# Optimization experiments

Measured on AMD Instinct MI355X. Metric: run time of the kernel, lower is better.

The kernel has to match this reference:

```python
import jax, jax.numpy as jnp
import numpy as np

B, N, D, C = 256, 256, 512, 1024
EPS = 1e-12  # F.normalize eps


def _l2norm(x):
    n = jnp.linalg.norm(x, axis=-1, keepdims=True)
    return x / jnp.maximum(n, EPS)


def setup_inputs() -> dict:
    key = jax.random.key(0)
    k1, k2, k3 = jax.random.split(key, 3)
    return {
        "image_tokens": jax.random.normal(k1, (B, N, D), dtype=jnp.float32),
        "text_features": jax.random.normal(k2, (C, D), dtype=jnp.float32),
        "log_tau": jnp.asarray(np.log(0.07), dtype=jnp.float32),
        "log_attn_tau": jnp.asarray(np.log(0.07), dtype=jnp.float32),
        "pid_labels": jax.random.randint(k3, (B,), 0, C),
    }


def reference(image_tokens, text_features, log_tau, log_attn_tau, pid_labels):
    toks = _l2norm(image_tokens.astype(jnp.float32))        # [B,N,D]
    txt = _l2norm(text_features.astype(jnp.float32))        # [C,D]
    sims = jnp.einsum('bnd,cd->bnc', toks, txt)             # [B,N,C]
    gt = pid_labels.astype(jnp.int32)
    # sims[arange(B), :, gt] -> [B,N]
    sims_gt = jnp.take_along_axis(sims, gt[:, None, None], axis=2)[..., 0]
    attn_tau = jnp.clip(jnp.exp(log_attn_tau), 0.01, 1.0)
    w = jax.nn.softmax(sims_gt / attn_tau, axis=1)          # [B,N]
    logits = jnp.einsum('bn,bnc->bc', w, sims)              # [B,C]
    tau = jnp.clip(jnp.exp(log_tau), 0.01, 1.0)
    logits = logits / tau
    # cross_entropy with label_smoothing=0.0, mean reduction
    logp = jax.nn.log_softmax(logits, axis=-1)
    nll = -jnp.take_along_axis(logp, gt[:, None], axis=1)[:, 0]
    return jnp.mean(nll)
```

## Files before the change

### kernel.cpp

```cpp
#include <hip/hip_runtime.h>
#include <math.h>

#define Bb 256
#define Nn 256
#define Dd 512
#define Cc 1024
#define KC 8
#define KD (Dd / KC)
#define PR 16
#define PSTR 516

__device__ __forceinline__ float waveReduceSum(float v) {
    #pragma unroll
    for (int off = 32; off > 0; off >>= 1)
        v += __shfl_xor(v, off, 64);
    return v;
}
__device__ __forceinline__ float waveReduceMax(float v) {
    #pragma unroll
    for (int off = 32; off > 0; off >>= 1)
        v = fmaxf(v, __shfl_xor(v, off, 64));
    return v;
}

__global__ void k_prep(const float* __restrict__ txt, float* __restrict__ txt_t,
                       float* __restrict__ invc) {
    __shared__ float tile[PR * PSTR];
    __shared__ float invs[PR];
    const int c0 = blockIdx.x * PR;
    const int tid = threadIdx.x;
    #pragma unroll
    for (int i = tid; i < PR * 128; i += 256) {
        const int r = i >> 7, c4 = i & 127;
        const float4 v = *(const float4*)(txt + (size_t)(c0 + r) * Dd + c4 * 4);
        *(float4*)&tile[r * PSTR + c4 * 4] = v;
    }
    __syncthreads();
    {
        const int r = tid >> 4, k = tid & 15;
        float s = 0.f;
        #pragma unroll
        for (int i = 0; i < 32; ++i) {
            const float x = tile[r * PSTR + i * 16 + k];
            s = fmaf(x, x, s);
        }
        s += __shfl_xor(s, 1, 64);
        s += __shfl_xor(s, 2, 64);
        s += __shfl_xor(s, 4, 64);
        s += __shfl_xor(s, 8, 64);
        if (k == 0) {
            const float inv = 1.0f / fmaxf(sqrtf(s), 1e-12f);
            invs[r] = inv;
            invc[c0 + r] = inv;
        }
    }
    __syncthreads();
    {
        const int c = tid & 15;
        const int d0 = tid >> 4;
        const float inv = invs[c];
        #pragma unroll
        for (int d = d0; d < Dd; d += 16)
            txt_t[(size_t)d * Cc + c0 + c] = tile[c * PSTR + d] * inv;
    }
}

__global__ void __launch_bounds__(1024) k_attn_q(const float* __restrict__ toks,
                                                 const float* __restrict__ txt,
                                                 const float* __restrict__ invc,
                                                 const int* __restrict__ pid,
                                                 const float* __restrict__ log_attn_tau,
                                                 float* __restrict__ q) {
    const int b = blockIdx.x;
    const int tid = threadIdx.x;
    const int wv = tid >> 6;
    const int lane = tid & 63;
    __shared__ float xg[Dd];
    __shared__ float qpart_s[16][Dd];
    __shared__ float ms[16], Ss[16];
    const int g = pid[b];
    if (tid < Dd) xg[tid] = txt[(size_t)g * Dd + tid] * invc[g];
    __syncthreads();
    float at = expf(log_attn_tau[0]);
    at = fminf(fmaxf(at, 0.01f), 1.0f);
    const float iat = 1.0f / at;

    const float4 xg0 = *(const float4*)&xg[lane * 8];
    const float4 xg1 = *(const float4*)&xg[lane * 8 + 4];

    float m = -INFINITY, S = 0.0f;
    float qa[8] = {0.f, 0.f, 0.f, 0.f, 0.f, 0.f, 0.f, 0.f};

    const float* base = toks + ((size_t)b * Nn + wv * 16) * Dd + lane * 8;
    float4 t0 = *(const float4*)base;
    float4 t1 = *(const float4*)(base + 4);
    #pragma unroll 4
    for (int r = 0; r < 16; ++r) {
        float4 n0, n1;
        if (r < 15) {
            const float* p = base + (size_t)(r + 1) * Dd;
            n0 = *(const float4*)p;
            n1 = *(const float4*)(p + 4);
        }
        float dot = t0.x*xg0.x + t0.y*xg0.y + t0.z*xg0.z + t0.w*xg0.w
                  + t1.x*xg1.x + t1.y*xg1.y + t1.z*xg1.z + t1.w*xg1.w;
        float ss  = t0.x*t0.x + t0.y*t0.y + t0.z*t0.z + t0.w*t0.w
                  + t1.x*t1.x + t1.y*t1.y + t1.z*t1.z + t1.w*t1.w;
        dot = waveReduceSum(dot);
        ss = waveReduceSum(ss);
        const float inv = 1.0f / fmaxf(sqrtf(ss), 1e-12f);
        const float s = dot * inv;
        if (s > m) {
            const float sc = expf((m - s) * iat);
            S = S * sc + 1.0f;
            qa[0] = qa[0]*sc + inv*t0.x; qa[1] = qa[1]*sc + inv*t0.y;
            qa[2] = qa[2]*sc + inv*t0.z; qa[3] = qa[3]*sc + inv*t0.w;
            qa[4] = qa[4]*sc + inv*t1.x; qa[5] = qa[5]*sc + inv*t1.y;
            qa[6] = qa[6]*sc + inv*t1.z; qa[7] = qa[7]*sc + inv*t1.w;
            m = s;
        } else {
            const float e = expf((s - m) * iat);
            S += e;
            const float w = e * inv;
            qa[0] = fmaf(w, t0.x, qa[0]); qa[1] = fmaf(w, t0.y, qa[1]);
            qa[2] = fmaf(w, t0.z, qa[2]); qa[3] = fmaf(w, t0.w, qa[3]);
            qa[4] = fmaf(w, t1.x, qa[4]); qa[5] = fmaf(w, t1.y, qa[5]);
            qa[6] = fmaf(w, t1.z, qa[6]); qa[7] = fmaf(w, t1.w, qa[7]);
        }
        t0 = n0; t1 = n1;
    }
    #pragma unroll
    for (int j = 0; j < 8; ++j) qpart_s[wv][lane * 8 + j] = qa[j];
    if (lane == 0) { ms[wv] = m; Ss[wv] = S; }
    __syncthreads();
    if (tid < Dd) {
        float M = -INFINITY;
        #pragma unroll
        for (int w = 0; w < 16; ++w) M = fmaxf(M, ms[w]);
        float Stot = 0.f, acc = 0.f;
        #pragma unroll
        for (int w = 0; w < 16; ++w) {
            const float sc = expf((ms[w] - M) * iat);
            Stot = fmaf(Ss[w], sc, Stot);
            acc = fmaf(qpart_s[w][tid], sc, acc);
        }
        q[(size_t)b * Dd + tid] = acc / Stot;
    }
}

__global__ void k_logits(const float* __restrict__ q, const float* __restrict__ txt_t,
                         float* __restrict__ part) {
    const int b0 = blockIdx.x * 4;
    const int kc = blockIdx.y;
    const int d0 = kc * KD;
    const int t = threadIdx.x;
    __shared__ float qs[4][KD];
    {
        const int j = t >> 6, d = t & 63;
        qs[j][d] = q[(size_t)(b0 + j) * Dd + d0 + d];
    }
    __syncthreads();
    const float4* xt = (const float4*)txt_t;
    float4 a0 = {0,0,0,0}, a1 = {0,0,0,0}, a2 = {0,0,0,0}, a3 = {0,0,0,0};
    #pragma unroll 4
    for (int d = 0; d < KD; d += 4) {
        const float4 q0 = *(const float4*)&qs[0][d];
        const float4 q1 = *(const float4*)&qs[1][d];
        const float4 q2 = *(const float4*)&qs[2][d];
        const float4 q3 = *(const float4*)&qs[3][d];
        const float4 x0 = xt[(size_t)(d0 + d + 0) * (Cc / 4) + t];
        const float4 x1 = xt[(size_t)(d0 + d + 1) * (Cc / 4) + t];
        const float4 x2 = xt[(size_t)(d0 + d + 2) * (Cc / 4) + t];
        const float4 x3 = xt[(size_t)(d0 + d + 3) * (Cc / 4) + t];
        a0.x = fmaf(q0.x,x0.x,a0.x); a0.y = fmaf(q0.x,x0.y,a0.y); a0.z = fmaf(q0.x,x0.z,a0.z); a0.w = fmaf(q0.x,x0.w,a0.w);
        a0.x = fmaf(q0.y,x1.x,a0.x); a0.y = fmaf(q0.y,x1.y,a0.y); a0.z = fmaf(q0.y,x1.z,a0.z); a0.w = fmaf(q0.y,x1.w,a0.w);
        a0.x = fmaf(q0.z,x2.x,a0.x); a0.y = fmaf(q0.z,x2.y,a0.y); a0.z = fmaf(q0.z,x2.z,a0.z); a0.w = fmaf(q0.z,x2.w,a0.w);
        a0.x = fmaf(q0.w,x3.x,a0.x); a0.y = fmaf(q0.w,x3.y,a0.y); a0.z = fmaf(q0.w,x3.z,a0.z); a0.w = fmaf(q0.w,x3.w,a0.w);
        a1.x = fmaf(q1.x,x0.x,a1.x); a1.y = fmaf(q1.x,x0.y,a1.y); a1.z = fmaf(q1.x,x0.z,a1.z); a1.w = fmaf(q1.x,x0.w,a1.w);
        a1.x = fmaf(q1.y,x1.x,a1.x); a1.y = fmaf(q1.y,x1.y,a1.y); a1.z = fmaf(q1.y,x1.z,a1.z); a1.w = fmaf(q1.y,x1.w,a1.w);
        a1.x = fmaf(q1.z,x2.x,a1.x); a1.y = fmaf(q1.z,x2.y,a1.y); a1.z = fmaf(q1.z,x2.z,a1.z); a1.w = fmaf(q1.z,x2.w,a1.w);
        a1.x = fmaf(q1.w,x3.x,a1.x); a1.y = fmaf(q1.w,x3.y,a1.y); a1.z = fmaf(q1.w,x3.z,a1.z); a1.w = fmaf(q1.w,x3.w,a1.w);
        a2.x = fmaf(q2.x,x0.x,a2.x); a2.y = fmaf(q2.x,x0.y,a2.y); a2.z = fmaf(q2.x,x0.z,a2.z); a2.w = fmaf(q2.x,x0.w,a2.w);
        a2.x = fmaf(q2.y,x1.x,a2.x); a2.y = fmaf(q2.y,x1.y,a2.y); a2.z = fmaf(q2.y,x1.z,a2.z); a2.w = fmaf(q2.y,x1.w,a2.w);
        a2.x = fmaf(q2.z,x2.x,a2.x); a2.y = fmaf(q2.z,x2.y,a2.y); a2.z = fmaf(q2.z,x2.z,a2.z); a2.w = fmaf(q2.z,x2.w,a2.w);
        a2.x = fmaf(q2.w,x3.x,a2.x); a2.y = fmaf(q2.w,x3.y,a2.y); a2.z = fmaf(q2.w,x3.z,a2.z); a2.w = fmaf(q2.w,x3.w,a2.w);
        a3.x = fmaf(q3.x,x0.x,a3.x); a3.y = fmaf(q3.x,x0.y,a3.y); a3.z = fmaf(q3.x,x0.z,a3.z); a3.w = fmaf(q3.x,x0.w,a3.w);
        a3.x = fmaf(q3.y,x1.x,a3.x); a3.y = fmaf(q3.y,x1.y,a3.y); a3.z = fmaf(q3.y,x1.z,a3.z); a3.w = fmaf(q3.y,x1.w,a3.w);
        a3.x = fmaf(q3.z,x2.x,a3.x); a3.y = fmaf(q3.z,x2.y,a3.y); a3.z = fmaf(q3.z,x2.z,a3.z); a3.w = fmaf(q3.z,x2.w,a3.w);
        a3.x = fmaf(q3.w,x3.x,a3.x); a3.y = fmaf(q3.w,x3.y,a3.y); a3.z = fmaf(q3.w,x3.z,a3.z); a3.w = fmaf(q3.w,x3.w,a3.w);
    }
    float* pb = part + ((size_t)kc * Bb + b0) * Cc;
    ((float4*)(pb + 0 * Cc))[t] = a0;
    ((float4*)(pb + 1 * Cc))[t] = a1;
    ((float4*)(pb + 2 * Cc))[t] = a2;
    ((float4*)(pb + 3 * Cc))[t] = a3;
}

__global__ void k_lse(const float* __restrict__ part, const int* __restrict__ pid,
                      const float* __restrict__ log_tau, float* __restrict__ out) {
    const int b = blockIdx.x;
    const int t = threadIdx.x;
    float4 l = {0,0,0,0};
    #pragma unroll
    for (int kc = 0; kc < KC; ++kc) {
        const float4 p = ((const float4*)(part + ((size_t)kc * Bb + b) * Cc))[t];
        l.x += p.x; l.y += p.y; l.z += p.z; l.w += p.w;
    }
    float tau = expf(log_tau[0]);
    tau = fminf(fmaxf(tau, 0.01f), 1.0f);
    const float itau = 1.0f / tau;
    l.x *= itau; l.y *= itau; l.z *= itau; l.w *= itau;

    const int g = pid[b];
    __shared__ float redm[4], reds[4], sgt;
    if ((g >> 2) == t) {
        const float v[4] = {l.x, l.y, l.z, l.w};
        sgt = v[g & 3];
    }
    float m = fmaxf(fmaxf(l.x, l.y), fmaxf(l.z, l.w));
    m = waveReduceMax(m);
    if ((t & 63) == 0) redm[t >> 6] = m;
    __syncthreads();
    m = fmaxf(fmaxf(redm[0], redm[1]), fmaxf(redm[2], redm[3]));
    float e = expf(l.x - m) + expf(l.y - m) + expf(l.z - m) + expf(l.w - m);
    e = waveReduceSum(e);
    if ((t & 63) == 0) reds[t >> 6] = e;
    __syncthreads();
    if (t == 0) {
        const float S = reds[0] + reds[1] + reds[2] + reds[3];
        const float nll = m + logf(S) - sgt;
        atomicAdd(out, nll * (1.0f / (float)Bb));
    }
}

extern "C" void kernel_launch(void* const* d_in, const int* in_sizes, int n_in,
                              void* d_out, int out_size, void* d_ws, size_t ws_size,
                              hipStream_t stream) {
    const float* toks = (const float*)d_in[0];
    const float* txt = (const float*)d_in[1];
    const float* log_tau = (const float*)d_in[2];
    const float* log_attn_tau = (const float*)d_in[3];
    const int* pid = (const int*)d_in[4];
    float* out = (float*)d_out;

    float* ws = (float*)d_ws;
    float* txt_t = ws;
    float* invc  = txt_t + (size_t)Dd * Cc;
    float* q     = invc + Cc;
    float* part  = q + (size_t)Bb * Dd;

    hipMemsetAsync(out, 0, sizeof(float), stream);
    k_prep<<<Cc / PR, 256, 0, stream>>>(txt, txt_t, invc);
    k_attn_q<<<Bb, 1024, 0, stream>>>(toks, txt, invc, pid, log_attn_tau, q);
    k_logits<<<dim3(Bb / 4, KC), 256, 0, stream>>>(q, txt_t, part);
    k_lse<<<Bb, 256, 0, stream>>>(part, pid, log_tau, out);
}
```

Before: 222.6 us.

## Split attention pooling across two blocks per batch and decouple from text prep

```diff
diff --git a/kernel.cpp b/kernel.cpp
--- a/kernel.cpp
+++ b/kernel.cpp
@@ -7,7 +7,7 @@
 #define Cc 1024
 #define KC 8
 #define KD (Dd / KC)
-#define PR 16
+#define PR 32
 #define PSTR 516
 
 __device__ __forceinline__ float waveReduceSum(float v) {
@@ -23,8 +23,7 @@
     return v;
 }
 
-__global__ void k_prep(const float* __restrict__ txt, float* __restrict__ txt_t,
-                       float* __restrict__ invc) {
+__global__ void k_prep(const float* __restrict__ txt, float* __restrict__ txt_t) {
     __shared__ float tile[PR * PSTR];
     __shared__ float invs[PR];
     const int c0 = blockIdx.x * PR;
@@ -37,50 +36,56 @@
     }
     __syncthreads();
     {
-        const int r = tid >> 4, k = tid & 15;
+        const int r = tid >> 3, k = tid & 7;
         float s = 0.f;
         #pragma unroll
-        for (int i = 0; i < 32; ++i) {
-            const float x = tile[r * PSTR + i * 16 + k];
+        for (int i = 0; i < 64; ++i) {
+            const float x = tile[r * PSTR + i * 8 + k];
             s = fmaf(x, x, s);
         }
         s += __shfl_xor(s, 1, 64);
         s += __shfl_xor(s, 2, 64);
         s += __shfl_xor(s, 4, 64);
-        s += __shfl_xor(s, 8, 64);
-        if (k == 0) {
-            const float inv = 1.0f / fmaxf(sqrtf(s), 1e-12f);
-            invs[r] = inv;
-            invc[c0 + r] = inv;
-        }
-    }
-    __syncthreads();
-    {
-        const int c = tid & 15;
-        const int d0 = tid >> 4;
+        if (k == 0) invs[r] = 1.0f / fmaxf(sqrtf(s), 1e-12f);
+    }
+    __syncthreads();
+    {
+        const int c = tid & 31;
+        const int d0 = tid >> 5;
         const float inv = invs[c];
         #pragma unroll
-        for (int d = d0; d < Dd; d += 16)
+        for (int d = d0; d < Dd; d += 8)
             txt_t[(size_t)d * Cc + c0 + c] = tile[c * PSTR + d] * inv;
     }
 }
 
-__global__ void __launch_bounds__(1024) k_attn_q(const float* __restrict__ toks,
-                                                 const float* __restrict__ txt,
-                                                 const float* __restrict__ invc,
-                                                 const int* __restrict__ pid,
-                                                 const float* __restrict__ log_attn_tau,
-                                                 float* __restrict__ q) {
-    const int b = blockIdx.x;
+__global__ void __launch_bounds__(512) k_attn_q(const float* __restrict__ toks,
+                                                const float* __restrict__ txt,
+                                                const int* __restrict__ pid,
+                                                const float* __restrict__ log_attn_tau,
+                                                float* __restrict__ qp,
+                                                float2* __restrict__ mS) {
+    const int b = blockIdx.x >> 1;
+    const int half = blockIdx.x & 1;
     const int tid = threadIdx.x;
     const int wv = tid >> 6;
     const int lane = tid & 63;
     __shared__ float xg[Dd];
-    __shared__ float qpart_s[16][Dd];
-    __shared__ float ms[16], Ss[16];
+    __shared__ float qpart_s[8][Dd];
+    __shared__ float ms[8], Ss[8], ssw[8];
     const int g = pid[b];
-    if (tid < Dd) xg[tid] = txt[(size_t)g * Dd + tid] * invc[g];
-    __syncthreads();
+    {
+        const float x = txt[(size_t)g * Dd + tid];
+        xg[tid] = x;
+        float s = waveReduceSum(x * x);
+        if (lane == 0) ssw[wv] = s;
+    }
+    __syncthreads();
+    float ssg = 0.f;
+    #pragma unroll
+    for (int w = 0; w < 8; ++w) ssg += ssw[w];
+    const float invg = 1.0f / fmaxf(sqrtf(ssg), 1e-12f);
+
     float at = expf(log_attn_tau[0]);
     at = fminf(fmaxf(at, 0.01f), 1.0f);
     const float iat = 1.0f / at;
@@ -91,73 +96,93 @@
     float m = -INFINITY, S = 0.0f;
     float qa[8] = {0.f, 0.f, 0.f, 0.f, 0.f, 0.f, 0.f, 0.f};
 
-    const float* base = toks + ((size_t)b * Nn + wv * 16) * Dd + lane * 8;
-    float4 t0 = *(const float4*)base;
-    float4 t1 = *(const float4*)(base + 4);
+    const float* base = toks + ((size_t)b * Nn + half * 128 + wv * 16) * Dd + lane * 8;
+    float4 c0a = *(const float4*)base;
+    float4 c0b = *(const float4*)(base + 4);
+    float4 c1a = *(const float4*)(base + Dd);
+    float4 c1b = *(const float4*)(base + Dd + 4);
     #pragma unroll 4
     for (int r = 0; r < 16; ++r) {
-        float4 n0, n1;
-        if (r < 15) {
-            const float* p = base + (size_t)(r + 1) * Dd;
-            n0 = *(const float4*)p;
-            n1 = *(const float4*)(p + 4);
-        }
-        float dot = t0.x*xg0.x + t0.y*xg0.y + t0.z*xg0.z + t0.w*xg0.w
-                  + t1.x*xg1.x + t1.y*xg1.y + t1.z*xg1.z + t1.w*xg1.w;
-        float ss  = t0.x*t0.x + t0.y*t0.y + t0.z*t0.z + t0.w*t0.w
-                  + t1.x*t1.x + t1.y*t1.y + t1.z*t1.z + t1.w*t1.w;
+        float4 na, nb;
+        if (r < 14) {
+            const float* p = base + (size_t)(r + 2) * Dd;
+            na = *(const float4*)p;
+            nb = *(const float4*)(p + 4);
+        }
+        float dot = c0a.x*xg0.x + c0a.y*xg0.y + c0a.z*xg0.z + c0a.w*xg0.w
+                  + c0b.x*xg1.x + c0b.y*xg1.y + c0b.z*xg1.z + c0b.w*xg1.w;
+        float ss  = c0a.x*c0a.x + c0a.y*c0a.y + c0a.z*c0a.z + c0a.w*c0a.w
+                  + c0b.x*c0b.x + c0b.y*c0b.y + c0b.z*c0b.z + c0b.w*c0b.w;
         dot = waveReduceSum(dot);
         ss = waveReduceSum(ss);
         const float inv = 1.0f / fmaxf(sqrtf(ss), 1e-12f);
-        const float s = dot * inv;
+        const float s = dot * inv * invg;
         if (s > m) {
             const float sc = expf((m - s) * iat);
             S = S * sc + 1.0f;
-            qa[0] = qa[0]*sc + inv*t0.x; qa[1] = qa[1]*sc + inv*t0.y;
-            qa[2] = qa[2]*sc + inv*t0.z; qa[3] = qa[3]*sc + inv*t0.w;
-            qa[4] = qa[4]*sc + inv*t1.x; qa[5] = qa[5]*sc + inv*t1.y;
-            qa[6] = qa[6]*sc + inv*t1.z; qa[7] = qa[7]*sc + inv*t1.w;
+            qa[0] = qa[0]*sc + inv*c0a.x; qa[1] = qa[1]*sc + inv*c0a.y;
+            qa[2] = qa[2]*sc + inv*c0a.z; qa[3] = qa[3]*sc + inv*c0a.w;
+            qa[4] = qa[4]*sc + inv*c0b.x; qa[5] = qa[5]*sc + inv*c0b.y;
+            qa[6] = qa[6]*sc + inv*c0b.z; qa[7] = qa[7]*sc + inv*c0b.w;
             m = s;
         } else {
             const float e = expf((s - m) * iat);
             S += e;
             const float w = e * inv;
-            qa[0] = fmaf(w, t0.x, qa[0]); qa[1] = fmaf(w, t0.y, qa[1]);
-            qa[2] = fmaf(w, t0.z, qa[2]); qa[3] = fmaf(w, t0.w, qa[3]);
-            qa[4] = fmaf(w, t1.x, qa[4]); qa[5] = fmaf(w, t1.y, qa[5]);
-            qa[6] = fmaf(w, t1.z, qa[6]); qa[7] = fmaf(w, t1.w, qa[7]);
-        }
-        t0 = n0; t1 = n1;
+            qa[0] = fmaf(w, c0a.x, qa[0]); qa[1] = fmaf(w, c0a.y, qa[1]);
+            qa[2] = fmaf(w, c0a.z, qa[2]); qa[3] = fmaf(w, c0a.w, qa[3]);
+            qa[4] = fmaf(w, c0b.x, qa[4]); qa[5] = fmaf(w, c0b.y, qa[5]);
+            qa[6] = fmaf(w, c0b.z, qa[6]); qa[7] = fmaf(w, c0b.w, qa[7]);
+        }
+        c0a = c1a; c0b = c1b; c1a = na; c1b = nb;
     }
     #pragma unroll
     for (int j = 0; j < 8; ++j) qpart_s[wv][lane * 8 + j] = qa[j];
     if (lane == 0) { ms[wv] = m; Ss[wv] = S; }
     __syncthreads();
-    if (tid < Dd) {
+    {
         float M = -INFINITY;
         #pragma unroll
-        for (int w = 0; w < 16; ++w) M = fmaxf(M, ms[w]);
+        for (int w = 0; w < 8; ++w) M = fmaxf(M, ms[w]);
         float Stot = 0.f, acc = 0.f;
         #pragma unroll
-        for (int w = 0; w < 16; ++w) {
+        for (int w = 0; w < 8; ++w) {
             const float sc = expf((ms[w] - M) * iat);
             Stot = fmaf(Ss[w], sc, Stot);
             acc = fmaf(qpart_s[w][tid], sc, acc);
         }
-        q[(size_t)b * Dd + tid] = acc / Stot;
-    }
-}
-
-__global__ void k_logits(const float* __restrict__ q, const float* __restrict__ txt_t,
-                         float* __restrict__ part) {
+        qp[((size_t)b * 2 + half) * Dd + tid] = acc;
+        if (tid == 0) mS[b * 2 + half] = make_float2(M, Stot);
+    }
+}
+
+__global__ void k_logits(const float* __restrict__ qp, const float2* __restrict__ mS,
+                         const float* __restrict__ log_attn_tau,
+                         const float* __restrict__ txt_t, float* __restrict__ part) {
     const int b0 = blockIdx.x * 4;
     const int kc = blockIdx.y;
     const int d0 = kc * KD;
     const int t = threadIdx.x;
     __shared__ float qs[4][KD];
+    __shared__ float A0s[4], A1s[4], RSs[4];
+    if (t < 4) {
+        float at = expf(log_attn_tau[0]);
+        at = fminf(fmaxf(at, 0.01f), 1.0f);
+        const float iat = 1.0f / at;
+        const float2 h0 = mS[(b0 + t) * 2 + 0];
+        const float2 h1 = mS[(b0 + t) * 2 + 1];
+        const float M = fmaxf(h0.x, h1.x);
+        const float a0 = expf((h0.x - M) * iat);
+        const float a1 = expf((h1.x - M) * iat);
+        A0s[t] = a0; A1s[t] = a1;
+        RSs[t] = 1.0f / (h0.y * a0 + h1.y * a1);
+    }
+    __syncthreads();
     {
         const int j = t >> 6, d = t & 63;
-        qs[j][d] = q[(size_t)(b0 + j) * Dd + d0 + d];
+        const float v0 = qp[((size_t)(b0 + j) * 2 + 0) * Dd + d0 + d];
+        const float v1 = qp[((size_t)(b0 + j) * 2 + 1) * Dd + d0 + d];
+        qs[j][d] = (v0 * A0s[j] + v1 * A1s[j]) * RSs[j];
     }
     __syncthreads();
     const float4* xt = (const float4*)txt_t;
@@ -245,13 +270,13 @@
 
     float* ws = (float*)d_ws;
     float* txt_t = ws;
-    float* invc  = txt_t + (size_t)Dd * Cc;
-    float* q     = invc + Cc;
-    float* part  = q + (size_t)Bb * Dd;
+    float* qp    = txt_t + (size_t)Dd * Cc;
+    float2* mS   = (float2*)(qp + (size_t)Bb * 2 * Dd);
+    float* part  = (float*)(mS + Bb * 2);
 
     hipMemsetAsync(out, 0, sizeof(float), stream);
-    k_prep<<<Cc / PR, 256, 0, stream>>>(txt, txt_t, invc);
-    k_attn_q<<<Bb, 1024, 0, stream>>>(toks, txt, invc, pid, log_attn_tau, q);
-    k_logits<<<dim3(Bb / 4, KC), 256, 0, stream>>>(q, txt_t, part);
+    k_attn_q<<<Bb * 2, 512, 0, stream>>>(toks, txt, pid, log_attn_tau, qp, mS);
+    k_prep<<<Cc / PR, 256, 0, stream>>>(txt, txt_t);
+    k_logits<<<dim3(Bb / 4, KC), 256, 0, stream>>>(qp, mS, log_attn_tau, txt_t, part);
     k_lse<<<Bb, 256, 0, stream>>>(part, pid, log_tau, out);
 }
```

Measured after the change: 228.8 us. +2.8%, slower.
